# Kernel tuning notes

Hardware: AMD Instinct MI355X
Metric: run time of the kernel (lower is better)

## Reference

```python
import jax, jax.numpy as jnp
import numpy as np

B, LQ, D = 4, 10000, 256
HEADS, LVLS, PTS = 8, 1, 4
HW = 100
LIN = HW * HW


def setup_inputs() -> dict:
    key = jax.random.key(0)
    ks = jax.random.split(key, 14)
    s = 0.02
    ctr = jax.random.uniform(ks[2], (B, LQ, LVLS, 2), jnp.float32)
    wh = 0.05 + 0.2 * jax.random.uniform(ks[3], (B, LQ, LVLS, 2), jnp.float32)
    return {
        "query": jax.random.normal(ks[0], (B, LQ, D), jnp.float32),
        "reference_points": jnp.concatenate([ctr, wh], axis=-1),
        "input_flatten": jax.random.normal(ks[1], (B, LIN, D), jnp.float32),
        "input_spatial_shapes": jnp.array([[HW, HW]], jnp.int32),
        "input_level_start_index": jnp.zeros((LVLS,), jnp.int32),
        "input_padding_mask": jnp.zeros((B, LIN), jnp.bool_),
        "Wv": s * jax.random.normal(ks[4], (D, D), jnp.float32),
        "bv": jnp.zeros((D,), jnp.float32),
        "Woff": s * jax.random.normal(ks[5], (D, HEADS * LVLS * PTS * 2), jnp.float32),
        "boff": s * jax.random.normal(ks[6], (HEADS * LVLS * PTS * 2,), jnp.float32),
        "Wa": s * jax.random.normal(ks[7], (D, HEADS * LVLS * PTS), jnp.float32),
        "ba": jnp.zeros((HEADS * LVLS * PTS,), jnp.float32),
        "Wout": s * jax.random.normal(ks[8], (D, D), jnp.float32),
        "bout": jnp.zeros((D,), jnp.float32),
    }


def _ms_deform_attn(query, reference_points, input_flatten, input_padding_mask,
                    Wv, bv, Woff, boff, Wa, ba, Wout, bout):
    Bn, Lq, Dm = query.shape
    Lin = input_flatten.shape[1]
    Hh, L, P = HEADS, LVLS, PTS
    Cd = Dm // Hh
    # value projection + padding mask
    value = input_flatten @ Wv + bv
    value = jnp.where(input_padding_mask[..., None], 0.0, value)
    # sampling offsets & attention weights
    off = (query @ Woff + boff).reshape(Bn, Lq, Hh, L, P, 2)
    attn = jax.nn.softmax((query @ Wa + ba).reshape(Bn, Lq, Hh, L * P), axis=-1)
    loc = (reference_points[:, :, None, :, None, :2]
           + off / P * reference_points[:, :, None, :, None, 2:] * 0.5)
    # value -> (B*Hh, Cd, Lin); square single-level map H=W=sqrt(Lin)
    v = value.reshape(Bn, Lin, Hh, Cd).transpose(0, 2, 3, 1).reshape(Bn * Hh, Cd, Lin)
    Hs = int(round(Lin ** 0.5)); Ws = Hs
    # level 0 grid: (B*Hh, Lq, P, 2), normalized to [-1, 1]
    g = (2.0 * loc - 1.0)[:, :, :, 0].transpose(0, 2, 1, 3, 4).reshape(Bn * Hh, Lq, P, 2)
    x = (g[..., 0] + 1.0) * Ws / 2.0 - 0.5
    y = (g[..., 1] + 1.0) * Hs / 2.0 - 0.5
    x0 = jnp.floor(x).astype(jnp.int32); y0 = jnp.floor(y).astype(jnp.int32)
    x1 = x0 + 1; y1 = y0 + 1
    wx = x - x0.astype(x.dtype); wy = y - y0.astype(y.dtype)

    def valid(xi, yi):
        return ((xi >= 0) & (xi < Ws) & (yi >= 0) & (yi < Hs)).astype(value.dtype)

    def gather(xi, yi):
        idx = (jnp.clip(yi, 0, Hs - 1) * Ws + jnp.clip(xi, 0, Ws - 1)).reshape(Bn * Hh, 1, Lq * P)
        out = jnp.take_along_axis(v, jnp.broadcast_to(idx, (Bn * Hh, Cd, Lq * P)), axis=2)
        return out.reshape(Bn * Hh, Cd, Lq, P)

    sv = (gather(x0, y0) * ((1 - wx) * (1 - wy) * valid(x0, y0))[:, None]
          + gather(x0, y1) * ((1 - wx) * wy * valid(x0, y1))[:, None]
          + gather(x1, y0) * (wx * (1 - wy) * valid(x1, y0))[:, None]
          + gather(x1, y1) * (wx * wy * valid(x1, y1))[:, None])  # (B*Hh, Cd, Lq, P)
    aw = attn.transpose(0, 2, 1, 3).reshape(Bn * Hh, 1, Lq, L * P)
    out = (sv * aw).sum(-1).reshape(Bn, Hh * Cd, Lq).transpose(0, 2, 1)  # (B, Lq, D)
    return out @ Wout + bout


def reference(query, reference_points, input_flatten, input_spatial_shapes,
              input_level_start_index, input_padding_mask,
              Wv, bv, Woff, boff, Wa, ba, Wout, bout):
    # input_spatial_shapes / level_start_index are redundant here: the core is
    # single-level with H=W=sqrt(Len_in) (faithful to the source code).
    return _ms_deform_attn(query, reference_points, input_flatten, input_padding_mask,
                           Wv, bv, Woff, boff, Wa, ba, Wout, bout)
```

## Files before the change

### kernel.cpp

```cpp
#include <hip/hip_runtime.h>

#define BATCH 4
#define LQ    10000
#define DM    256
#define NH    8
#define NP    4
#define HWD   100
#define LIN   10000

typedef unsigned short ushort_t;
typedef __attribute__((ext_vector_type(8))) short bf16x8;
typedef __attribute__((ext_vector_type(8))) unsigned short u16x8;
typedef __attribute__((ext_vector_type(4))) float f32x4;

__device__ __forceinline__ unsigned short f2bf(float f) {
    unsigned int u = __float_as_uint(f);
    u += 0x7FFFu + ((u >> 16) & 1u);
    return (unsigned short)(u >> 16);
}

__global__ __launch_bounds__(256) void prep_kernel(
    const float* __restrict__ Wv, const float* __restrict__ Wout,
    const float* __restrict__ Woff, const float* __restrict__ Wa,
    const float* __restrict__ boff, const float* __restrict__ ba,
    ushort_t* __restrict__ WtV, ushort_t* __restrict__ WtO,
    ushort_t* __restrict__ Wcomb, float* __restrict__ bcomb)
{
    const int n = blockIdx.x, k = threadIdx.x;
    if (blockIdx.y == 0) {
        WtV[n * 256 + k] = f2bf(Wv[(size_t)k * 256 + n]);
    } else if (blockIdx.y == 1) {
        WtO[n * 256 + k] = f2bf(Wout[(size_t)k * 256 + n]);
    } else if (n < 96) {
        float w = (n < 64) ? Woff[(size_t)k * 64 + n] : Wa[(size_t)k * 32 + (n - 64)];
        Wcomb[n * 256 + k] = f2bf(w);
        if (k == 0) bcomb[n] = (n < 64) ? boff[n] : ba[n - 64];
    }
}

__global__ __launch_bounds__(256) void gemm_in_kernel(
    const float* __restrict__ flat, const float* __restrict__ query,
    const ushort_t* __restrict__ WtV, const ushort_t* __restrict__ Wcomb,
    const float* __restrict__ bv, const float* __restrict__ bcomb,
    ushort_t* __restrict__ value, float* __restrict__ oaproj)
{
    __shared__ ushort_t As[64 * 32];
    __shared__ ushort_t Bs[256 * 32];

    const int tid  = threadIdx.x;
    const int lane = tid & 63;
    const int wv   = tid >> 6;

    const int ar  = tid >> 2;
    const int akb = tid & 3;
    const int asw = (akb ^ ((ar >> 1) & 3)) * 8;
    const int fr = lane & 15, kb = lane >> 4;

    if (blockIdx.x < 625) {
        const int row0 = blockIdx.x * 64;
        const f32x4 zero = {0.f, 0.f, 0.f, 0.f};
        f32x4 acc[4][4];
        #pragma unroll
        for (int m = 0; m < 4; ++m)
            #pragma unroll
            for (int n = 0; n < 4; ++n) acc[m][n] = zero;

        for (int k0 = 0; k0 < 256; k0 += 32) {
            {
                const float* p = &flat[(size_t)(row0 + ar) * 256 + k0 + akb * 8];
                float4 f0 = *reinterpret_cast<const float4*>(p);
                float4 f1 = *reinterpret_cast<const float4*>(p + 4);
                u16x8 pk;
                pk[0] = f2bf(f0.x); pk[1] = f2bf(f0.y);
                pk[2] = f2bf(f0.z); pk[3] = f2bf(f0.w);
                pk[4] = f2bf(f1.x); pk[5] = f2bf(f1.y);
                pk[6] = f2bf(f1.z); pk[7] = f2bf(f1.w);
                *reinterpret_cast<u16x8*>(&As[ar * 32 + asw]) = pk;
            }
            #pragma unroll
            for (int j = 0; j < 4; ++j) {
                int n = (tid >> 2) + 64 * j;
                uint4 v = *reinterpret_cast<const uint4*>(
                    &WtV[(size_t)n * 256 + k0 + akb * 8]);
                *reinterpret_cast<uint4*>(
                    &Bs[n * 32 + ((akb ^ ((n >> 1) & 3)) * 8)]) = v;
            }
            __syncthreads();

            bf16x8 af[4], bf[4];
            #pragma unroll
            for (int m = 0; m < 4; ++m) {
                int r = m * 16 + fr;
                af[m] = *reinterpret_cast<const bf16x8*>(
                    &As[r * 32 + ((kb ^ ((r >> 1) & 3)) * 8)]);
            }
            #pragma unroll
            for (int n = 0; n < 4; ++n) {
                int c = wv * 64 + n * 16 + fr;
                bf[n] = *reinterpret_cast<const bf16x8*>(
                    &Bs[c * 32 + ((kb ^ ((c >> 1) & 3)) * 8)]);
            }
            #pragma unroll
            for (int m = 0; m < 4; ++m)
                #pragma unroll
                for (int n = 0; n < 4; ++n)
                    acc[m][n] = __builtin_amdgcn_mfma_f32_16x16x32_bf16(
                        af[m], bf[n], acc[m][n], 0, 0, 0);
            __syncthreads();
        }

        #pragma unroll
        for (int n = 0; n < 4; ++n) {
            int c = wv * 64 + n * 16 + fr;
            float bb = bv[c];
            int hh = c >> 5, ch = c & 31;
            #pragma unroll
            for (int m = 0; m < 4; ++m) {
                #pragma unroll
                for (int j = 0; j < 4; ++j) {
                    int r = row0 + m * 16 + kb * 4 + j;
                    int rb = (int)((unsigned)r / 10000u);
                    int pix = r - rb * 10000;
                    size_t addr = (((size_t)(rb * 8 + hh)) * LIN + pix) * 32 + ch;
                    value[addr] = f2bf(acc[m][n][j] + bb);
                }
            }
        }
    } else {
        const int row0 = (blockIdx.x - 625) * 64;
        const f32x4 zero = {0.f, 0.f, 0.f, 0.f};
        f32x4 acc[6];
        #pragma unroll
        for (int n = 0; n < 6; ++n) acc[n] = zero;

        for (int k0 = 0; k0 < 256; k0 += 32) {
            {
                const float* p = &query[(size_t)(row0 + ar) * 256 + k0 + akb * 8];
                float4 f0 = *reinterpret_cast<const float4*>(p);
                float4 f1 = *reinterpret_cast<const float4*>(p + 4);
                u16x8 pk;
                pk[0] = f2bf(f0.x); pk[1] = f2bf(f0.y);
                pk[2] = f2bf(f0.z); pk[3] = f2bf(f0.w);
                pk[4] = f2bf(f1.x); pk[5] = f2bf(f1.y);
                pk[6] = f2bf(f1.z); pk[7] = f2bf(f1.w);
                *reinterpret_cast<u16x8*>(&As[ar * 32 + asw]) = pk;
            }
            #pragma unroll
            for (int j = 0; j < 2; ++j) {
                int n = (tid >> 2) + 64 * j;
                if (n < 96) {
                    uint4 v = *reinterpret_cast<const uint4*>(
                        &Wcomb[(size_t)n * 256 + k0 + akb * 8]);
                    *reinterpret_cast<uint4*>(
                        &Bs[n * 32 + ((akb ^ ((n >> 1) & 3)) * 8)]) = v;
                }
            }
            __syncthreads();

            bf16x8 af;
            {
                int r = wv * 16 + fr;
                af = *reinterpret_cast<const bf16x8*>(
                    &As[r * 32 + ((kb ^ ((r >> 1) & 3)) * 8)]);
            }
            #pragma unroll
            for (int n = 0; n < 6; ++n) {
                int c = n * 16 + fr;
                bf16x8 bf = *reinterpret_cast<const bf16x8*>(
                    &Bs[c * 32 + ((kb ^ ((c >> 1) & 3)) * 8)]);
                acc[n] = __builtin_amdgcn_mfma_f32_16x16x32_bf16(
                    af, bf, acc[n], 0, 0, 0);
            }
            __syncthreads();
        }

        #pragma unroll
        for (int n = 0; n < 6; ++n) {
            int c = n * 16 + fr;
            float bb = bcomb[c];
            #pragma unroll
            for (int j = 0; j < 4; ++j) {
                int r = row0 + wv * 16 + kb * 4 + j;
                oaproj[(size_t)r * 96 + c] = acc[n][j] + bb;
            }
        }
    }
}

__global__ __launch_bounds__(256, 4) void deform_kernel(
    const float* __restrict__ oaproj, const float* __restrict__ refpts,
    const ushort_t* __restrict__ value, ushort_t* __restrict__ out)
{
    __shared__ int4   soff[NP * 64];
    __shared__ float4 swt [NP * 64];

    const int blk = blockIdx.x;
    const int xcd = blk & 7;
    const int sub = (blk >> 3) & 3;
    const int chunk = blk >> 5;
    const int map = xcd * 4 + sub;
    const int b = map >> 3, h = map & 7;
    const int q0 = chunk * 64;

    const int tid = threadIdx.x;

    if (tid < 64) {
        const int qg = q0 + tid;
        if (qg >= LQ) {
            int4 zi = {0, 0, 0, 0};
            float4 zf = {0.f, 0.f, 0.f, 0.f};
            #pragma unroll
            for (int p = 0; p < NP; ++p) { soff[p * 64 + tid] = zi; swt[p * 64 + tid] = zf; }
        } else {
            const size_t row = (size_t)b * LQ + qg;
            const float* oa = oaproj + row * 96;
            float4 l4 = *reinterpret_cast<const float4*>(oa + 64 + h * 4);
            float mx = fmaxf(fmaxf(l4.x, l4.y), fmaxf(l4.z, l4.w));
            float e0 = __expf(l4.x - mx), e1 = __expf(l4.y - mx);
            float e2 = __expf(l4.z - mx), e3 = __expf(l4.w - mx);
            float inv = 1.f / (e0 + e1 + e2 + e3);
            float ew[4] = {e0 * inv, e1 * inv, e2 * inv, e3 * inv};
            float4 o0 = *reinterpret_cast<const float4*>(oa + h * 8);
            float4 o1 = *reinterpret_cast<const float4*>(oa + h * 8 + 4);
            float oxv[4] = {o0.x, o0.z, o1.x, o1.z};
            float oyv[4] = {o0.y, o0.w, o1.y, o1.w};
            const float* rp = refpts + row * 4;
            float cx = rp[0], cy = rp[1], rw = rp[2], rh = rp[3];
            #pragma unroll
            for (int p = 0; p < NP; ++p) {
                float x = (cx + oxv[p] * rw * 0.125f) * (float)HWD - 0.5f;
                float y = (cy + oyv[p] * rh * 0.125f) * (float)HWD - 0.5f;
                float x0f = floorf(x), y0f = floorf(y);
                float wx = x - x0f, wy = y - y0f;
                int x0 = (int)x0f, y0 = (int)y0f;
                int x1 = x0 + 1, y1 = y0 + 1;
                float vx0 = (x0 >= 0 && x0 < HWD) ? 1.f : 0.f;
                float vx1 = (x1 >= 0 && x1 < HWD) ? 1.f : 0.f;
                float vy0 = (y0 >= 0 && y0 < HWD) ? 1.f : 0.f;
                float vy1 = (y1 >= 0 && y1 < HWD) ? 1.f : 0.f;
                int cx0 = min(max(x0, 0), HWD - 1), cx1 = min(max(x1, 0), HWD - 1);
                int cy0 = min(max(y0, 0), HWD - 1), cy1 = min(max(y1, 0), HWD - 1);
                float aw = ew[p];
                int4 of = {cy0 * HWD + cx0, cy0 * HWD + cx1,
                           cy1 * HWD + cx0, cy1 * HWD + cx1};
                float4 wt = {aw * (1.f - wx) * (1.f - wy) * vx0 * vy0,
                             aw * wx * (1.f - wy) * vx1 * vy0,
                             aw * (1.f - wx) * wy * vx0 * vy1,
                             aw * wx * wy * vx1 * vy1};
                soff[p * 64 + tid] = of;
                swt [p * 64 + tid] = wt;
            }
        }
    }
    __syncthreads();

    const int q = tid >> 2, c8 = tid & 3;
    const int qg = q0 + q;
    const ushort_t* vb = value + (size_t)map * (LIN * 32) + c8 * 8;

    int4 of[4]; float4 w4[4];
    #pragma unroll
    for (int p = 0; p < NP; ++p) {
        of[p] = soff[p * 64 + q];
        w4[p] = swt [p * 64 + q];
    }
    uint4 vv[4][4];
    #pragma unroll
    for (int p = 0; p < NP; ++p) {
        vv[p][0] = *reinterpret_cast<const uint4*>(vb + ((size_t)of[p].x << 5));
        vv[p][1] = *reinterpret_cast<const uint4*>(vb + ((size_t)of[p].y << 5));
        vv[p][2] = *reinterpret_cast<const uint4*>(vb + ((size_t)of[p].z << 5));
        vv[p][3] = *reinterpret_cast<const uint4*>(vb + ((size_t)of[p].w << 5));
    }
    float a0 = 0.f, a1 = 0.f, a2 = 0.f, a3 = 0.f;
    float a4 = 0.f, a5 = 0.f, a6 = 0.f, a7 = 0.f;
    #define ACC(V, W) { const float w_ = (W); const uint4 v_ = (V); \
        a0 += w_ * __uint_as_float(v_.x << 16); \
        a1 += w_ * __uint_as_float(v_.x & 0xffff0000u); \
        a2 += w_ * __uint_as_float(v_.y << 16); \
        a3 += w_ * __uint_as_float(v_.y & 0xffff0000u); \
        a4 += w_ * __uint_as_float(v_.z << 16); \
        a5 += w_ * __uint_as_float(v_.z & 0xffff0000u); \
        a6 += w_ * __uint_as_float(v_.w << 16); \
        a7 += w_ * __uint_as_float(v_.w & 0xffff0000u); }
    #pragma unroll
    for (int p = 0; p < NP; ++p) {
        ACC(vv[p][0], w4[p].x);
        ACC(vv[p][1], w4[p].y);
        ACC(vv[p][2], w4[p].z);
        ACC(vv[p][3], w4[p].w);
    }
    #undef ACC

    if (qg < LQ) {
        const size_t orow = (size_t)b * LQ + qg;
        u16x8 pk;
        pk[0] = f2bf(a0); pk[1] = f2bf(a1);
        pk[2] = f2bf(a2); pk[3] = f2bf(a3);
        pk[4] = f2bf(a4); pk[5] = f2bf(a5);
        pk[6] = f2bf(a6); pk[7] = f2bf(a7);
        *reinterpret_cast<u16x8*>(&out[orow * 256 + h * 32 + c8 * 8]) = pk;
    }
}

__global__ __launch_bounds__(256) void gemm_out_kernel(
    const ushort_t* __restrict__ A, const ushort_t* __restrict__ Wt,
    const float* __restrict__ bias, float* __restrict__ Cout)
{
    __shared__ ushort_t As[64 * 32];
    __shared__ ushort_t Bs[256 * 32];

    const int tid  = threadIdx.x;
    const int lane = tid & 63;
    const int wv   = tid >> 6;
    const int row0 = blockIdx.x * 64;

    const f32x4 zero = {0.f, 0.f, 0.f, 0.f};
    f32x4 acc[4][4];
    #pragma unroll
    for (int m = 0; m < 4; ++m)
        #pragma unroll
        for (int n = 0; n < 4; ++n) acc[m][n] = zero;

    const int ar  = tid >> 2;
    const int akb = tid & 3;
    const int asw = (akb ^ ((ar >> 1) & 3)) * 8;
    const int fr = lane & 15, kb = lane >> 4;

    for (int k0 = 0; k0 < 256; k0 += 32) {
        {
            uint4 v = *reinterpret_cast<const uint4*>(
                &A[(size_t)(row0 + ar) * 256 + k0 + akb * 8]);
            *reinterpret_cast<uint4*>(&As[ar * 32 + asw]) = v;
        }
        #pragma unroll
        for (int j = 0; j < 4; ++j) {
            int n = (tid >> 2) + 64 * j;
            uint4 v = *reinterpret_cast<const uint4*>(
                &Wt[(size_t)n * 256 + k0 + akb * 8]);
            *reinterpret_cast<uint4*>(
                &Bs[n * 32 + ((akb ^ ((n >> 1) & 3)) * 8)]) = v;
        }
        __syncthreads();

        bf16x8 af[4], bf[4];
        #pragma unroll
        for (int m = 0; m < 4; ++m) {
            int r = m * 16 + fr;
            af[m] = *reinterpret_cast<const bf16x8*>(
                &As[r * 32 + ((kb ^ ((r >> 1) & 3)) * 8)]);
        }
        #pragma unroll
        for (int n = 0; n < 4; ++n) {
            int c = wv * 64 + n * 16 + fr;
            bf[n] = *reinterpret_cast<const bf16x8*>(
                &Bs[c * 32 + ((kb ^ ((c >> 1) & 3)) * 8)]);
        }
        #pragma unroll
        for (int m = 0; m < 4; ++m)
            #pragma unroll
            for (int n = 0; n < 4; ++n)
                acc[m][n] = __builtin_amdgcn_mfma_f32_16x16x32_bf16(
                    af[m], bf[n], acc[m][n], 0, 0, 0);
        __syncthreads();
    }

    #pragma unroll
    for (int m = 0; m < 4; ++m) {
        #pragma unroll
        for (int n = 0; n < 4; ++n) {
            int c = wv * 64 + n * 16 + fr;
            float bb = bias[c];
            #pragma unroll
            for (int j = 0; j < 4; ++j) {
                int r = row0 + m * 16 + kb * 4 + j;
                Cout[(size_t)r * 256 + c] = acc[m][n][j] + bb;
            }
        }
    }
}

extern "C" void kernel_launch(void* const* d_in, const int* in_sizes, int n_in,
                              void* d_out, int out_size, void* d_ws, size_t ws_size,
                              hipStream_t stream)
{
    const float* query  = (const float*)d_in[0];
    const float* refpts = (const float*)d_in[1];
    const float* flat   = (const float*)d_in[2];
    const float* Wv   = (const float*)d_in[6];
    const float* bv   = (const float*)d_in[7];
    const float* Woff = (const float*)d_in[8];
    const float* boff = (const float*)d_in[9];
    const float* Wa   = (const float*)d_in[10];
    const float* ba   = (const float*)d_in[11];
    const float* Wout = (const float*)d_in[12];
    const float* bout = (const float*)d_in[13];
    float* out = (float*)d_out;

    const size_t MROWS = (size_t)BATCH * LIN;
    ushort_t* value  = (ushort_t*)d_ws;
    ushort_t* ws2    = value + MROWS * DM;
    ushort_t* WtV    = ws2 + MROWS * DM;
    ushort_t* WtO    = WtV + 256 * 256;
    ushort_t* Wcomb  = WtO + 256 * 256;
    float*    bcomb  = (float*)(Wcomb + 96 * 256);
    float*    oaproj = bcomb + 128;

    dim3 blk(256);

    prep_kernel<<<dim3(256, 3), blk, 0, stream>>>(
        Wv, Wout, Woff, Wa, boff, ba, WtV, WtO, Wcomb, bcomb);

    gemm_in_kernel<<<dim3(1250), blk, 0, stream>>>(
        flat, query, WtV, Wcomb, bv, bcomb, value, oaproj);

    deform_kernel<<<dim3(157 * 32), blk, 0, stream>>>(
        oaproj, refpts, value, ws2);

    gemm_out_kernel<<<dim3(MROWS / 64), blk, 0, stream>>>(
        ws2, WtO, bout, out);
}
```

Baseline: 84.31 us.

## Use direct global-to-LDS loads with pre-swizzled weights and K=64 tiles

The weight matrices are written in an XOR-swizzled global layout by the prep kernel, and the deform kernel writes its bf16 output in the same swizzled layout. The GEMMs can then stage tiles with global_load_lds straight into shared memory, skipping the register round-trip. The K tile doubles from 32 to 64, halving the loop iterations and barriers. In exchange, shared memory per block doubles, which may lower occupancy, and the layout contract between the kernels becomes implicit.

```diff
diff --git a/kernel.cpp b/kernel.cpp
--- a/kernel.cpp
+++ b/kernel.cpp
@@ -17,6 +17,12 @@
     unsigned int u = __float_as_uint(f);
     u += 0x7FFFu + ((u >> 16) & 1u);
     return (unsigned short)(u >> 16);
+}
+
+__device__ __forceinline__ void gload16(const ushort_t* g, ushort_t* l) {
+    __builtin_amdgcn_global_load_lds(
+        (const __attribute__((address_space(1))) void*)g,
+        (__attribute__((address_space(3))) void*)l, 16, 0, 0);
 }
 
 __global__ __launch_bounds__(256) void prep_kernel(
@@ -27,13 +33,16 @@
     ushort_t* __restrict__ Wcomb, float* __restrict__ bcomb)
 {
     const int n = blockIdx.x, k = threadIdx.x;
+    const int t = k >> 6, lc = (k >> 3) & 7, j = k & 7;
+    const int ct = lc ^ ((n >> 1) & 7);
+    const size_t addr = (size_t)n * 256 + t * 64 + ct * 8 + j;
     if (blockIdx.y == 0) {
-        WtV[n * 256 + k] = f2bf(Wv[(size_t)k * 256 + n]);
+        WtV[addr] = f2bf(Wv[(size_t)k * 256 + n]);
     } else if (blockIdx.y == 1) {
-        WtO[n * 256 + k] = f2bf(Wout[(size_t)k * 256 + n]);
+        WtO[addr] = f2bf(Wout[(size_t)k * 256 + n]);
     } else if (n < 96) {
         float w = (n < 64) ? Woff[(size_t)k * 64 + n] : Wa[(size_t)k * 32 + (n - 64)];
-        Wcomb[n * 256 + k] = f2bf(w);
+        Wcomb[addr] = f2bf(w);
         if (k == 0) bcomb[n] = (n < 64) ? boff[n] : ba[n - 64];
     }
 }
@@ -44,8 +53,8 @@
     const float* __restrict__ bv, const float* __restrict__ bcomb,
     ushort_t* __restrict__ value, float* __restrict__ oaproj)
 {
-    __shared__ ushort_t As[64 * 32];
-    __shared__ ushort_t Bs[256 * 32];
+    __shared__ ushort_t As[64 * 64];
+    __shared__ ushort_t Bs[256 * 64];
 
     const int tid  = threadIdx.x;
     const int lane = tid & 63;
@@ -53,8 +62,9 @@
 
     const int ar  = tid >> 2;
     const int akb = tid & 3;
-    const int asw = (akb ^ ((ar >> 1) & 3)) * 8;
+    const int as_ = (ar >> 1) & 7;
     const int fr = lane & 15, kb = lane >> 4;
+    const int ln8 = lane >> 3, lc8 = lane & 7;
 
     if (blockIdx.x < 625) {
         const int row0 = blockIdx.x * 64;
@@ -65,7 +75,14 @@
             #pragma unroll
             for (int n = 0; n < 4; ++n) acc[m][n] = zero;
 
-        for (int k0 = 0; k0 < 256; k0 += 32) {
+        for (int k0 = 0; k0 < 256; k0 += 64) {
+            const int t = k0 >> 6;
+            #pragma unroll
+            for (int it = 0; it < 8; ++it) {
+                int r0 = (it * 4 + wv) * 8;
+                gload16(&WtV[(size_t)(r0 + ln8) * 256 + t * 64 + lc8 * 8],
+                        &Bs[r0 * 64]);
+            }
             {
                 const float* p = &flat[(size_t)(row0 + ar) * 256 + k0 + akb * 8];
                 float4 f0 = *reinterpret_cast<const float4*>(p);
@@ -75,37 +92,40 @@
                 pk[2] = f2bf(f0.z); pk[3] = f2bf(f0.w);
                 pk[4] = f2bf(f1.x); pk[5] = f2bf(f1.y);
                 pk[6] = f2bf(f1.z); pk[7] = f2bf(f1.w);
-                *reinterpret_cast<u16x8*>(&As[ar * 32 + asw]) = pk;
-            }
-            #pragma unroll
-            for (int j = 0; j < 4; ++j) {
-                int n = (tid >> 2) + 64 * j;
-                uint4 v = *reinterpret_cast<const uint4*>(
-                    &WtV[(size_t)n * 256 + k0 + akb * 8]);
-                *reinterpret_cast<uint4*>(
-                    &Bs[n * 32 + ((akb ^ ((n >> 1) & 3)) * 8)]) = v;
+                *reinterpret_cast<u16x8*>(&As[ar * 64 + ((akb ^ as_) * 8)]) = pk;
+                f0 = *reinterpret_cast<const float4*>(p + 32);
+                f1 = *reinterpret_cast<const float4*>(p + 36);
+                pk[0] = f2bf(f0.x); pk[1] = f2bf(f0.y);
+                pk[2] = f2bf(f0.z); pk[3] = f2bf(f0.w);
+                pk[4] = f2bf(f1.x); pk[5] = f2bf(f1.y);
+                pk[6] = f2bf(f1.z); pk[7] = f2bf(f1.w);
+                *reinterpret_cast<u16x8*>(&As[ar * 64 + (((akb + 4) ^ as_) * 8)]) = pk;
             }
             __syncthreads();
 
-            bf16x8 af[4], bf[4];
-            #pragma unroll
-            for (int m = 0; m < 4; ++m) {
-                int r = m * 16 + fr;
-                af[m] = *reinterpret_cast<const bf16x8*>(
-                    &As[r * 32 + ((kb ^ ((r >> 1) & 3)) * 8)]);
-            }
-            #pragma unroll
-            for (int n = 0; n < 4; ++n) {
-                int c = wv * 64 + n * 16 + fr;
-                bf[n] = *reinterpret_cast<const bf16x8*>(
-                    &Bs[c * 32 + ((kb ^ ((c >> 1) & 3)) * 8)]);
-            }
-            #pragma unroll
-            for (int m = 0; m < 4; ++m)
-                #pragma unroll
-                for (int n = 0; n < 4; ++n)
-                    acc[m][n] = __builtin_amdgcn_mfma_f32_16x16x32_bf16(
-                        af[m], bf[n], acc[m][n], 0, 0, 0);
+            #pragma unroll
+            for (int ks = 0; ks < 2; ++ks) {
+                const int lc = ks * 4 + kb;
+                bf16x8 af[4], bf[4];
+                #pragma unroll
+                for (int m = 0; m < 4; ++m) {
+                    int r = m * 16 + fr;
+                    af[m] = *reinterpret_cast<const bf16x8*>(
+                        &As[r * 64 + ((lc ^ ((r >> 1) & 7)) * 8)]);
+                }
+                #pragma unroll
+                for (int n = 0; n < 4; ++n) {
+                    int c = wv * 64 + n * 16 + fr;
+                    bf[n] = *reinterpret_cast<const bf16x8*>(
+                        &Bs[c * 64 + ((lc ^ ((c >> 1) & 7)) * 8)]);
+                }
+                #pragma unroll
+                for (int m = 0; m < 4; ++m)
+                    #pragma unroll
+                    for (int n = 0; n < 4; ++n)
+                        acc[m][n] = __builtin_amdgcn_mfma_f32_16x16x32_bf16(
+                            af[m], bf[n], acc[m][n], 0, 0, 0);
+            }
             __syncthreads();
         }
 
@@ -133,7 +153,14 @@
         #pragma unroll
         for (int n = 0; n < 6; ++n) acc[n] = zero;
 
-        for (int k0 = 0; k0 < 256; k0 += 32) {
+        for (int k0 = 0; k0 < 256; k0 += 64) {
+            const int t = k0 >> 6;
+            #pragma unroll
+            for (int it = 0; it < 3; ++it) {
+                int r0 = (it * 4 + wv) * 8;
+                gload16(&Wcomb[(size_t)(r0 + ln8) * 256 + t * 64 + lc8 * 8],
+                        &Bs[r0 * 64]);
+            }
             {
                 const float* p = &query[(size_t)(row0 + ar) * 256 + k0 + akb * 8];
                 float4 f0 = *reinterpret_cast<const float4*>(p);
@@ -143,33 +170,34 @@
                 pk[2] = f2bf(f0.z); pk[3] = f2bf(f0.w);
                 pk[4] = f2bf(f1.x); pk[5] = f2bf(f1.y);
                 pk[6] = f2bf(f1.z); pk[7] = f2bf(f1.w);
-                *reinterpret_cast<u16x8*>(&As[ar * 32 + asw]) = pk;
-            }
-            #pragma unroll
-            for (int j = 0; j < 2; ++j) {
-                int n = (tid >> 2) + 64 * j;
-                if (n < 96) {
-                    uint4 v = *reinterpret_cast<const uint4*>(
-                        &Wcomb[(size_t)n * 256 + k0 + akb * 8]);
-                    *reinterpret_cast<uint4*>(
-                        &Bs[n * 32 + ((akb ^ ((n >> 1) & 3)) * 8)]) = v;
+                *reinterpret_cast<u16x8*>(&As[ar * 64 + ((akb ^ as_) * 8)]) = pk;
+                f0 = *reinterpret_cast<const float4*>(p + 32);
+                f1 = *reinterpret_cast<const float4*>(p + 36);
+                pk[0] = f2bf(f0.x); pk[1] = f2bf(f0.y);
+                pk[2] = f2bf(f0.z); pk[3] = f2bf(f0.w);
+                pk[4] = f2bf(f1.x); pk[5] = f2bf(f1.y);
+                pk[6] = f2bf(f1.z); pk[7] = f2bf(f1.w);
+                *reinterpret_cast<u16x8*>(&As[ar * 64 + (((akb + 4) ^ as_) * 8)]) = pk;
+            }
+            __syncthreads();
+
+            #pragma unroll
+            for (int ks = 0; ks < 2; ++ks) {
+                const int lc = ks * 4 + kb;
+                bf16x8 af;
+                {
+                    int r = wv * 16 + fr;
+                    af = *reinterpret_cast<const bf16x8*>(
+                        &As[r * 64 + ((lc ^ ((r >> 1) & 7)) * 8)]);
                 }
-            }
-            __syncthreads();
-
-            bf16x8 af;
-            {
-                int r = wv * 16 + fr;
-                af = *reinterpret_cast<const bf16x8*>(
-                    &As[r * 32 + ((kb ^ ((r >> 1) & 3)) * 8)]);
-            }
-            #pragma unroll
-            for (int n = 0; n < 6; ++n) {
-                int c = n * 16 + fr;
-                bf16x8 bf = *reinterpret_cast<const bf16x8*>(
-                    &Bs[c * 32 + ((kb ^ ((c >> 1) & 3)) * 8)]);
-                acc[n] = __builtin_amdgcn_mfma_f32_16x16x32_bf16(
-                    af, bf, acc[n], 0, 0, 0);
+                #pragma unroll
+                for (int n = 0; n < 6; ++n) {
+                    int c = n * 16 + fr;
+                    bf16x8 bf = *reinterpret_cast<const bf16x8*>(
+                        &Bs[c * 64 + ((lc ^ ((c >> 1) & 7)) * 8)]);
+                    acc[n] = __builtin_amdgcn_mfma_f32_16x16x32_bf16(
+                        af, bf, acc[n], 0, 0, 0);
+                }
             }
             __syncthreads();
         }
@@ -299,7 +327,10 @@
         pk[2] = f2bf(a2); pk[3] = f2bf(a3);
         pk[4] = f2bf(a4); pk[5] = f2bf(a5);
         pk[6] = f2bf(a6); pk[7] = f2bf(a7);
-        *reinterpret_cast<u16x8*>(&out[orow * 256 + h * 32 + c8 * 8]) = pk;
+        const int cc = h * 4 + c8;
+        const int t = cc >> 3;
+        const int ct = (cc & 7) ^ ((int)(orow >> 1) & 7);
+        *reinterpret_cast<u16x8*>(&out[orow * 256 + t * 64 + ct * 8]) = pk;
     }
 }
 
@@ -307,8 +338,8 @@
     const ushort_t* __restrict__ A, const ushort_t* __restrict__ Wt,
     const float* __restrict__ bias, float* __restrict__ Cout)
 {
-    __shared__ ushort_t As[64 * 32];
-    __shared__ ushort_t Bs[256 * 32];
+    __shared__ ushort_t As[64 * 64];
+    __shared__ ushort_t Bs[256 * 64];
 
     const int tid  = threadIdx.x;
     const int lane = tid & 63;
@@ -322,46 +353,48 @@
         #pragma unroll
         for (int n = 0; n < 4; ++n) acc[m][n] = zero;
 
-    const int ar  = tid >> 2;
-    const int akb = tid & 3;
-    const int asw = (akb ^ ((ar >> 1) & 3)) * 8;
     const int fr = lane & 15, kb = lane >> 4;
-
-    for (int k0 = 0; k0 < 256; k0 += 32) {
-        {
-            uint4 v = *reinterpret_cast<const uint4*>(
-                &A[(size_t)(row0 + ar) * 256 + k0 + akb * 8]);
-            *reinterpret_cast<uint4*>(&As[ar * 32 + asw]) = v;
-        }
-        #pragma unroll
-        for (int j = 0; j < 4; ++j) {
-            int n = (tid >> 2) + 64 * j;
-            uint4 v = *reinterpret_cast<const uint4*>(
-                &Wt[(size_t)n * 256 + k0 + akb * 8]);
-            *reinterpret_cast<uint4*>(
-                &Bs[n * 32 + ((akb ^ ((n >> 1) & 3)) * 8)]) = v;
+    const int ln8 = lane >> 3, lc8 = lane & 7;
+
+    for (int k0 = 0; k0 < 256; k0 += 64) {
+        const int t = k0 >> 6;
+        #pragma unroll
+        for (int it = 0; it < 2; ++it) {
+            int r0 = (it * 4 + wv) * 8;
+            gload16(&A[(size_t)(row0 + r0 + ln8) * 256 + t * 64 + lc8 * 8],
+                    &As[r0 * 64]);
+        }
+        #pragma unroll
+        for (int it = 0; it < 8; ++it) {
+            int r0 = (it * 4 + wv) * 8;
+            gload16(&Wt[(size_t)(r0 + ln8) * 256 + t * 64 + lc8 * 8],
+                    &Bs[r0 * 64]);
         }
         __syncthreads();
 
-        bf16x8 af[4], bf[4];
-        #pragma unroll
-        for (int m = 0; m < 4; ++m) {
-            int r = m * 16 + fr;
-            af[m] = *reinterpret_cast<const bf16x8*>(
-                &As[r * 32 + ((kb ^ ((r >> 1) & 3)) * 8)]);
-        }
-        #pragma unroll
-        for (int n = 0; n < 4; ++n) {
-            int c = wv * 64 + n * 16 + fr;
-            bf[n] = *reinterpret_cast<const bf16x8*>(
-                &Bs[c * 32 + ((kb ^ ((c >> 1) & 3)) * 8)]);
-        }
-        #pragma unroll
-        for (int m = 0; m < 4; ++m)
-            #pragma unroll
-            for (int n = 0; n < 4; ++n)
-                acc[m][n] = __builtin_amdgcn_mfma_f32_16x16x32_bf16(
-                    af[m], bf[n], acc[m][n], 0, 0, 0);
+        #pragma unroll
+        for (int ks = 0; ks < 2; ++ks) {
+            const int lc = ks * 4 + kb;
+            bf16x8 af[4], bf[4];
+            #pragma unroll
+            for (int m = 0; m < 4; ++m) {
+                int r = m * 16 + fr;
+                af[m] = *reinterpret_cast<const bf16x8*>(
+                    &As[r * 64 + ((lc ^ ((r >> 1) & 7)) * 8)]);
+            }
+            #pragma unroll
+            for (int n = 0; n < 4; ++n) {
+                int c = wv * 64 + n * 16 + fr;
+                bf[n] = *reinterpret_cast<const bf16x8*>(
+                    &Bs[c * 64 + ((lc ^ ((c >> 1) & 7)) * 8)]);
+            }
+            #pragma unroll
+            for (int m = 0; m < 4; ++m)
+                #pragma unroll
+                for (int n = 0; n < 4; ++n)
+                    acc[m][n] = __builtin_amdgcn_mfma_f32_16x16x32_bf16(
+                        af[m], bf[n], acc[m][n], 0, 0, 0);
+        }
         __syncthreads();
     }
 
```

Result: faster. 72.71 us (-13.8%).

## Load GEMM MFMA fragments directly from global memory, dropping LDS staging

Applied to the files above, without the earlier changes.

The input and output projection GEMMs no longer stage A and B tiles through shared memory with barriers. Each lane now loads its MFMA fragments straight from global memory, and the K loop is fully unrolled. This removes the LDS writes and reads and the __syncthreads calls. In exchange, each wave of a block re-reads the A rows from global or L2 instead of sharing them, and the fp32 activations are converted to bf16 redundantly across waves.

```diff
diff --git a/kernel.cpp b/kernel.cpp
--- a/kernel.cpp
+++ b/kernel.cpp
@@ -17,6 +17,15 @@
     unsigned int u = __float_as_uint(f);
     u += 0x7FFFu + ((u >> 16) & 1u);
     return (unsigned short)(u >> 16);
+}
+
+__device__ __forceinline__ bf16x8 pack8bf(float4 f0, float4 f1) {
+    bf16x8 pk;
+    pk[0] = (short)f2bf(f0.x); pk[1] = (short)f2bf(f0.y);
+    pk[2] = (short)f2bf(f0.z); pk[3] = (short)f2bf(f0.w);
+    pk[4] = (short)f2bf(f1.x); pk[5] = (short)f2bf(f1.y);
+    pk[6] = (short)f2bf(f1.z); pk[7] = (short)f2bf(f1.w);
+    return pk;
 }
 
 __global__ __launch_bounds__(256) void prep_kernel(
@@ -44,76 +53,55 @@
     const float* __restrict__ bv, const float* __restrict__ bcomb,
     ushort_t* __restrict__ value, float* __restrict__ oaproj)
 {
-    __shared__ ushort_t As[64 * 32];
-    __shared__ ushort_t Bs[256 * 32];
-
     const int tid  = threadIdx.x;
     const int lane = tid & 63;
     const int wv   = tid >> 6;
-
-    const int ar  = tid >> 2;
-    const int akb = tid & 3;
-    const int asw = (akb ^ ((ar >> 1) & 3)) * 8;
     const int fr = lane & 15, kb = lane >> 4;
+
+    const f32x4 zero = {0.f, 0.f, 0.f, 0.f};
 
     if (blockIdx.x < 625) {
         const int row0 = blockIdx.x * 64;
-        const f32x4 zero = {0.f, 0.f, 0.f, 0.f};
+        const float* apm[4];
+        #pragma unroll
+        for (int m = 0; m < 4; ++m)
+            apm[m] = &flat[(size_t)(row0 + m * 16 + fr) * 256 + kb * 8];
+        const ushort_t* bpn[4];
+        #pragma unroll
+        for (int n = 0; n < 4; ++n)
+            bpn[n] = &WtV[(size_t)(wv * 64 + n * 16 + fr) * 256 + kb * 8];
+
         f32x4 acc[4][4];
         #pragma unroll
         for (int m = 0; m < 4; ++m)
             #pragma unroll
             for (int n = 0; n < 4; ++n) acc[m][n] = zero;
 
-        for (int k0 = 0; k0 < 256; k0 += 32) {
-            {
-                const float* p = &flat[(size_t)(row0 + ar) * 256 + k0 + akb * 8];
-                float4 f0 = *reinterpret_cast<const float4*>(p);
-                float4 f1 = *reinterpret_cast<const float4*>(p + 4);
-                u16x8 pk;
-                pk[0] = f2bf(f0.x); pk[1] = f2bf(f0.y);
-                pk[2] = f2bf(f0.z); pk[3] = f2bf(f0.w);
-                pk[4] = f2bf(f1.x); pk[5] = f2bf(f1.y);
-                pk[6] = f2bf(f1.z); pk[7] = f2bf(f1.w);
-                *reinterpret_cast<u16x8*>(&As[ar * 32 + asw]) = pk;
-            }
-            #pragma unroll
-            for (int j = 0; j < 4; ++j) {
-                int n = (tid >> 2) + 64 * j;
-                uint4 v = *reinterpret_cast<const uint4*>(
-                    &WtV[(size_t)n * 256 + k0 + akb * 8]);
-                *reinterpret_cast<uint4*>(
-                    &Bs[n * 32 + ((akb ^ ((n >> 1) & 3)) * 8)]) = v;
-            }
-            __syncthreads();
-
+        #pragma unroll
+        for (int t = 0; t < 8; ++t) {
             bf16x8 af[4], bf[4];
             #pragma unroll
             for (int m = 0; m < 4; ++m) {
-                int r = m * 16 + fr;
-                af[m] = *reinterpret_cast<const bf16x8*>(
-                    &As[r * 32 + ((kb ^ ((r >> 1) & 3)) * 8)]);
-            }
-            #pragma unroll
-            for (int n = 0; n < 4; ++n) {
-                int c = wv * 64 + n * 16 + fr;
-                bf[n] = *reinterpret_cast<const bf16x8*>(
-                    &Bs[c * 32 + ((kb ^ ((c >> 1) & 3)) * 8)]);
-            }
+                float4 f0 = *reinterpret_cast<const float4*>(apm[m] + t * 32);
+                float4 f1 = *reinterpret_cast<const float4*>(apm[m] + t * 32 + 4);
+                af[m] = pack8bf(f0, f1);
+            }
+            #pragma unroll
+            for (int n = 0; n < 4; ++n)
+                bf[n] = *reinterpret_cast<const bf16x8*>(bpn[n] + t * 32);
             #pragma unroll
             for (int m = 0; m < 4; ++m)
                 #pragma unroll
                 for (int n = 0; n < 4; ++n)
                     acc[m][n] = __builtin_amdgcn_mfma_f32_16x16x32_bf16(
                         af[m], bf[n], acc[m][n], 0, 0, 0);
-            __syncthreads();
         }
 
         #pragma unroll
         for (int n = 0; n < 4; ++n) {
-            int c = wv * 64 + n * 16 + fr;
-            float bb = bv[c];
-            int hh = c >> 5, ch = c & 31;
+            int cc = wv * 64 + n * 16 + fr;
+            float bb = bv[cc];
+            int hh = cc >> 5, ch = cc & 31;
             #pragma unroll
             for (int m = 0; m < 4; ++m) {
                 #pragma unroll
@@ -128,60 +116,37 @@
         }
     } else {
         const int row0 = (blockIdx.x - 625) * 64;
-        const f32x4 zero = {0.f, 0.f, 0.f, 0.f};
+        const float* ap = &query[(size_t)(row0 + wv * 16 + fr) * 256 + kb * 8];
+        const ushort_t* bpn[6];
+        #pragma unroll
+        for (int n = 0; n < 6; ++n)
+            bpn[n] = &Wcomb[(size_t)(n * 16 + fr) * 256 + kb * 8];
+
         f32x4 acc[6];
         #pragma unroll
         for (int n = 0; n < 6; ++n) acc[n] = zero;
 
-        for (int k0 = 0; k0 < 256; k0 += 32) {
-            {
-                const float* p = &query[(size_t)(row0 + ar) * 256 + k0 + akb * 8];
-                float4 f0 = *reinterpret_cast<const float4*>(p);
-                float4 f1 = *reinterpret_cast<const float4*>(p + 4);
-                u16x8 pk;
-                pk[0] = f2bf(f0.x); pk[1] = f2bf(f0.y);
-                pk[2] = f2bf(f0.z); pk[3] = f2bf(f0.w);
-                pk[4] = f2bf(f1.x); pk[5] = f2bf(f1.y);
-                pk[6] = f2bf(f1.z); pk[7] = f2bf(f1.w);
-                *reinterpret_cast<u16x8*>(&As[ar * 32 + asw]) = pk;
-            }
-            #pragma unroll
-            for (int j = 0; j < 2; ++j) {
-                int n = (tid >> 2) + 64 * j;
-                if (n < 96) {
-                    uint4 v = *reinterpret_cast<const uint4*>(
-                        &Wcomb[(size_t)n * 256 + k0 + akb * 8]);
-                    *reinterpret_cast<uint4*>(
-                        &Bs[n * 32 + ((akb ^ ((n >> 1) & 3)) * 8)]) = v;
-                }
-            }
-            __syncthreads();
-
-            bf16x8 af;
-            {
-                int r = wv * 16 + fr;
-                af = *reinterpret_cast<const bf16x8*>(
-                    &As[r * 32 + ((kb ^ ((r >> 1) & 3)) * 8)]);
-            }
+        #pragma unroll
+        for (int t = 0; t < 8; ++t) {
+            float4 f0 = *reinterpret_cast<const float4*>(ap + t * 32);
+            float4 f1 = *reinterpret_cast<const float4*>(ap + t * 32 + 4);
+            bf16x8 af = pack8bf(f0, f1);
             #pragma unroll
             for (int n = 0; n < 6; ++n) {
-                int c = n * 16 + fr;
-                bf16x8 bf = *reinterpret_cast<const bf16x8*>(
-                    &Bs[c * 32 + ((kb ^ ((c >> 1) & 3)) * 8)]);
+                bf16x8 bf = *reinterpret_cast<const bf16x8*>(bpn[n] + t * 32);
                 acc[n] = __builtin_amdgcn_mfma_f32_16x16x32_bf16(
                     af, bf, acc[n], 0, 0, 0);
             }
-            __syncthreads();
         }
 
         #pragma unroll
         for (int n = 0; n < 6; ++n) {
-            int c = n * 16 + fr;
-            float bb = bcomb[c];
+            int cc = n * 16 + fr;
+            float bb = bcomb[cc];
             #pragma unroll
             for (int j = 0; j < 4; ++j) {
                 int r = row0 + wv * 16 + kb * 4 + j;
-                oaproj[(size_t)r * 96 + c] = acc[n][j] + bb;
+                oaproj[(size_t)r * 96 + cc] = acc[n][j] + bb;
             }
         }
     }
@@ -307,13 +272,20 @@
     const ushort_t* __restrict__ A, const ushort_t* __restrict__ Wt,
     const float* __restrict__ bias, float* __restrict__ Cout)
 {
-    __shared__ ushort_t As[64 * 32];
-    __shared__ ushort_t Bs[256 * 32];
-
     const int tid  = threadIdx.x;
     const int lane = tid & 63;
     const int wv   = tid >> 6;
     const int row0 = blockIdx.x * 64;
+    const int fr = lane & 15, kb = lane >> 4;
+
+    const ushort_t* apm[4];
+    #pragma unroll
+    for (int m = 0; m < 4; ++m)
+        apm[m] = &A[(size_t)(row0 + m * 16 + fr) * 256 + kb * 8];
+    const ushort_t* bpn[4];
+    #pragma unroll
+    for (int n = 0; n < 4; ++n)
+        bpn[n] = &Wt[(size_t)(wv * 64 + n * 16 + fr) * 256 + kb * 8];
 
     const f32x4 zero = {0.f, 0.f, 0.f, 0.f};
     f32x4 acc[4][4];
@@ -322,59 +294,33 @@
         #pragma unroll
         for (int n = 0; n < 4; ++n) acc[m][n] = zero;
 
-    const int ar  = tid >> 2;
-    const int akb = tid & 3;
-    const int asw = (akb ^ ((ar >> 1) & 3)) * 8;
-    const int fr = lane & 15, kb = lane >> 4;
-
-    for (int k0 = 0; k0 < 256; k0 += 32) {
-        {
-            uint4 v = *reinterpret_cast<const uint4*>(
-                &A[(size_t)(row0 + ar) * 256 + k0 + akb * 8]);
-            *reinterpret_cast<uint4*>(&As[ar * 32 + asw]) = v;
-        }
-        #pragma unroll
-        for (int j = 0; j < 4; ++j) {
-            int n = (tid >> 2) + 64 * j;
-            uint4 v = *reinterpret_cast<const uint4*>(
-                &Wt[(size_t)n * 256 + k0 + akb * 8]);
-            *reinterpret_cast<uint4*>(
-                &Bs[n * 32 + ((akb ^ ((n >> 1) & 3)) * 8)]) = v;
-        }
-        __syncthreads();
-
+    #pragma unroll
+    for (int t = 0; t < 8; ++t) {
         bf16x8 af[4], bf[4];
         #pragma unroll
-        for (int m = 0; m < 4; ++m) {
-            int r = m * 16 + fr;
-            af[m] = *reinterpret_cast<const bf16x8*>(
-                &As[r * 32 + ((kb ^ ((r >> 1) & 3)) * 8)]);
-        }
-        #pragma unroll
-        for (int n = 0; n < 4; ++n) {
-            int c = wv * 64 + n * 16 + fr;
-            bf[n] = *reinterpret_cast<const bf16x8*>(
-                &Bs[c * 32 + ((kb ^ ((c >> 1) & 3)) * 8)]);
-        }
+        for (int m = 0; m < 4; ++m)
+            af[m] = *reinterpret_cast<const bf16x8*>(apm[m] + t * 32);
+        #pragma unroll
+        for (int n = 0; n < 4; ++n)
+            bf[n] = *reinterpret_cast<const bf16x8*>(bpn[n] + t * 32);
         #pragma unroll
         for (int m = 0; m < 4; ++m)
             #pragma unroll
             for (int n = 0; n < 4; ++n)
                 acc[m][n] = __builtin_amdgcn_mfma_f32_16x16x32_bf16(
                     af[m], bf[n], acc[m][n], 0, 0, 0);
-        __syncthreads();
     }
 
     #pragma unroll
     for (int m = 0; m < 4; ++m) {
         #pragma unroll
         for (int n = 0; n < 4; ++n) {
-            int c = wv * 64 + n * 16 + fr;
-            float bb = bias[c];
+            int cc = wv * 64 + n * 16 + fr;
+            float bb = bias[cc];
             #pragma unroll
             for (int j = 0; j < 4; ++j) {
                 int r = row0 + m * 16 + kb * 4 + j;
-                Cout[(size_t)r * 256 + c] = acc[m][n][j] + bb;
+                Cout[(size_t)r * 256 + cc] = acc[m][n][j] + bb;
             }
         }
     }
```

New measurement: 114.1 us. 35.3% more time.
